# Kernel optimization log

Measured on AMD Instinct MI355X. Metric: run time of the kernel, lower is better.

Reference implementation:

```python
import jax, jax.numpy as jnp
import numpy as np

EMBED = 512
HEADS = 8
HEAD_DIM = EMBED // HEADS


def setup_inputs() -> dict:
    key = jax.random.key(0)
    ks = jax.random.split(key, 11)
    B, S, E = 2, 4096, EMBED
    scale = 1.0 / np.sqrt(E)
    inp = {
        "q": jax.random.normal(ks[0], (B, S, E), dtype=jnp.float32),
        "k": jax.random.normal(ks[1], (B, S, E), dtype=jnp.float32),
        "v": jax.random.normal(ks[2], (B, S, E), dtype=jnp.float32),
        # linear layer params (torch nn.Linear: y = x @ W.T + b)
        "Wq": jax.random.normal(ks[3], (E, E), dtype=jnp.float32) * scale,
        "bq": jnp.zeros((E,), dtype=jnp.float32),
        "Wk": jax.random.normal(ks[4], (E, E), dtype=jnp.float32) * scale,
        "bk": jnp.zeros((E,), dtype=jnp.float32),
        "Wv": jax.random.normal(ks[5], (E, E), dtype=jnp.float32) * scale,
        "bv": jnp.zeros((E,), dtype=jnp.float32),
        "Wo": jax.random.normal(ks[6], (E, E), dtype=jnp.float32) * scale,
        "bo": jnp.zeros((E,), dtype=jnp.float32),
    }
    return inp


def reference(q, k, v, Wq, bq, Wk, bk, Wv, bv, Wo, bo):
    B, Sq, E = q.shape
    Sk = k.shape[1]
    H, D = HEADS, HEAD_DIM
    # projections, split heads: [B, S, H, D]
    qh = (q @ Wq.T + bq).reshape(B, Sq, H, D)
    kh = (k @ Wk.T + bk).reshape(B, Sk, H, D)
    vh = (v @ Wv.T + bv).reshape(B, Sk, H, D)
    # full score matrix [B, H, Sq, Sk]; note: scaled by sqrt(embed_size), matching source
    scores = jnp.einsum('bqhe,bkhe->bhqk', qh, kh) / jnp.sqrt(jnp.float32(E))
    probs = jax.nn.softmax(scores, axis=-1)
    attn = jnp.einsum('bhql,blhd->bqhd', probs, vh)  # [B, Sq, H, D]
    concat = attn.reshape(B, Sq, E)
    return concat @ Wo.T + bo
```

## Files before the change

kernel.cpp:

```cpp
#include <hip/hip_runtime.h>
#include <hip/hip_bf16.h>

#define DEVFN __device__ __forceinline__

typedef __attribute__((ext_vector_type(8))) __bf16 bf16x8;
typedef __attribute__((ext_vector_type(4))) float f32x4;
typedef __attribute__((ext_vector_type(16))) float f32x16;

constexpr int E  = 512;
constexpr int S  = 4096;
constexpr int HD = 64;
constexpr int RT = 8192;

DEVFN unsigned int cvt_pk_bf16(float lo, float hi) {
  unsigned int r;
  asm("v_cvt_pk_bf16_f32 %0, %1, %2" : "=v"(r) : "v"(lo), "v"(hi));
  return r;
}
DEVFN void plswap(unsigned int& a, unsigned int& b) {
  asm("v_permlane32_swap_b32 %0, %1" : "+v"(a), "+v"(b));
}
DEVFN float ex2(float x) { return __builtin_amdgcn_exp2f(x); }

DEVFN unsigned short f2bf(float f) {
  union { float f; unsigned int u; } v; v.f = f;
  unsigned int u = v.u;
  return (unsigned short)((u + 0x7fffu + ((u >> 16) & 1u)) >> 16);
}

DEVFN f32x4 mfma16(bf16x8 a, bf16x8 b, f32x4 c) {
  return __builtin_amdgcn_mfma_f32_16x16x32_bf16(a, b, c, 0, 0, 0);
}
DEVFN f32x16 mfma32(bf16x8 a, bf16x8 b, f32x16 c) {
  return __builtin_amdgcn_mfma_f32_32x32x16_bf16(a, b, c, 0, 0, 0);
}

DEVFN uint4 pk8(const float4& a, const float4& b) {
  uint4 r;
  r.x = cvt_pk_bf16(a.x, a.y); r.y = cvt_pk_bf16(a.z, a.w);
  r.z = cvt_pk_bf16(b.x, b.y); r.w = cvt_pk_bf16(b.z, b.w);
  return r;
}
DEVFN bf16x8 asbf(uint4 u) { union { uint4 a; bf16x8 b; } c; c.a = u; return c.b; }

template<typename TIN, int OMODE>
DEVFN void gemm_body(const TIN* __restrict__ X, const float* __restrict__ W,
                     const float* __restrict__ bias, void* __restrict__ outp,
                     float scale, unsigned short (*Al)[72], unsigned short (*Bl)[72]) {
  const int bid0 = blockIdx.x;
  const int bid = ((bid0 & 7) << 5) | (bid0 >> 3);
  const int bm = bid >> 2, bn = bid & 3;
  const int tid = threadIdx.x;
  const int w = tid >> 6, lane = tid & 63;
  const int g = lane >> 4, ln = lane & 15;
  const int wm = w >> 2, wn = w & 3;
  const int r0 = bm * 128, n0 = bn * 128;
  const int srw = tid >> 2, sc0 = (tid & 3) * 16;

  f32x4 acc[4][2] = {};

  float4 af[4];
  uint4  au[2];
  float4 bp[4];

  auto loadA = [&](int k0) {
    if constexpr (sizeof(TIN) == 4) {
      const float* src = (const float*)X + (size_t)(r0 + srw) * E + k0 + sc0;
      #pragma unroll
      for (int i = 0; i < 4; ++i) af[i] = *(const float4*)(src + i * 4);
    } else {
      const unsigned short* src = (const unsigned short*)X + (size_t)(r0 + srw) * E + k0 + sc0;
      #pragma unroll
      for (int i = 0; i < 2; ++i) au[i] = *(const uint4*)(src + i * 8);
    }
  };
  auto loadB = [&](int k0) {
    const float* src = W + (size_t)(n0 + srw) * E + k0 + sc0;
    #pragma unroll
    for (int i = 0; i < 4; ++i) bp[i] = *(const float4*)(src + i * 4);
  };

  loadA(0); loadB(0);

  for (int k0 = 0; k0 < E; k0 += 64) {
    if constexpr (sizeof(TIN) == 4) {
      *(uint4*)&Al[srw][sc0]     = pk8(af[0], af[1]);
      *(uint4*)&Al[srw][sc0 + 8] = pk8(af[2], af[3]);
    } else {
      *(uint4*)&Al[srw][sc0]     = au[0];
      *(uint4*)&Al[srw][sc0 + 8] = au[1];
    }
    *(uint4*)&Bl[srw][sc0]     = pk8(bp[0], bp[1]);
    *(uint4*)&Bl[srw][sc0 + 8] = pk8(bp[2], bp[3]);
    __syncthreads();
    if (k0 + 64 < E) { loadA(k0 + 64); loadB(k0 + 64); }

    __builtin_amdgcn_s_setprio(1);
    #pragma unroll
    for (int kk = 0; kk < 2; ++kk) {
      bf16x8 afr[4], bfr[2];
      #pragma unroll
      for (int i = 0; i < 4; ++i)
        afr[i] = *(const bf16x8*)&Al[wm*64 + i*16 + ln][kk*32 + 8*g];
      #pragma unroll
      for (int j = 0; j < 2; ++j)
        bfr[j] = *(const bf16x8*)&Bl[wn*32 + j*16 + ln][kk*32 + 8*g];
      #pragma unroll
      for (int i = 0; i < 4; ++i)
        #pragma unroll
        for (int j = 0; j < 2; ++j)
          acc[i][j] = mfma16(afr[i], bfr[j], acc[i][j]);
    }
    __builtin_amdgcn_s_setprio(0);
    __syncthreads();
  }

  #pragma unroll
  for (int j = 0; j < 2; ++j) {
    const int gcol = n0 + wn*32 + j*16 + ln;
    const float bv = bias[gcol];
    #pragma unroll
    for (int i = 0; i < 4; ++i) {
      const int gr = r0 + wm*64 + i*16 + 4*g;
      #pragma unroll
      for (int r = 0; r < 4; ++r) {
        const float v = (acc[i][j][r] + bv) * scale;
        if constexpr (OMODE == 1)
          ((float*)outp)[(size_t)(gr + r) * E + gcol] = v;
        else if constexpr (OMODE == 0)
          ((unsigned short*)outp)[(size_t)(gr + r) * E + gcol] = f2bf(v);
        else
          ((unsigned short*)outp)[((size_t)((gr + r) >> 12) * E + gcol) * S + ((gr + r) & (S - 1))] = f2bf(v);
      }
    }
  }
}

__global__ __launch_bounds__(512) void gemm_qkv(const float* __restrict__ q,
    const float* __restrict__ k, const float* __restrict__ v,
    const float* __restrict__ Wq, const float* __restrict__ bq,
    const float* __restrict__ Wk, const float* __restrict__ bk,
    const float* __restrict__ Wv, const float* __restrict__ bv,
    unsigned short* qh, unsigned short* kh, unsigned short* vhT, float qscale) {
  __shared__ unsigned short Al[128][72];
  __shared__ unsigned short Bl[128][72];
  const int y = blockIdx.y;
  if (y == 0)      gemm_body<float, 0>(q, Wq, bq, qh, qscale, Al, Bl);
  else if (y == 1) gemm_body<float, 0>(k, Wk, bk, kh, 1.0f, Al, Bl);
  else             gemm_body<float, 2>(v, Wv, bv, vhT, 1.0f, Al, Bl);
}

__global__ __launch_bounds__(512) void gemm_o(const unsigned short* __restrict__ cc,
    const float* __restrict__ Wo, const float* __restrict__ bo, float* out) {
  __shared__ unsigned short Al[128][72];
  __shared__ unsigned short Bl[128][72];
  gemm_body<unsigned short, 1>(cc, Wo, bo, out, 1.0f, Al, Bl);
}

__global__ __launch_bounds__(512, 4) void attn_fwd(const unsigned short* __restrict__ qh,
                                                   const unsigned short* __restrict__ kh,
                                                   const unsigned short* __restrict__ vhT,
                                                   unsigned short* __restrict__ cc) {
  __shared__ unsigned short SM[2][4][64][72];

  const int bid = blockIdx.x;
  const int swz = (bid & 7) * 64 + (bid >> 3);
  const int bh = swz >> 5, qt = swz & 31;
  const int b = bh >> 3, h = bh & 7;

  const int tid = threadIdx.x;
  const int wv = tid >> 6, lane = tid & 63;
  const int half = wv >> 2, w4 = wv & 3;
  const int l31 = lane & 31, hi = lane >> 5;

  const unsigned short* qb = qh + (size_t)b * S * E + h * HD;
  const unsigned short* kb = kh + (size_t)b * S * E + h * HD;
  const unsigned short* vb = vhT + ((size_t)b * E + h * HD) * S;
  const int q0 = qt * 128 + w4 * 32;
  const int tbase = half * (S / 2);

  bf16x8 qf[4];
  #pragma unroll
  for (int kf = 0; kf < 4; ++kf)
    qf[kf] = *(const bf16x8*)(qb + (size_t)(q0 + l31) * E + kf*16 + 8*hi);

  f32x16 o0 = {}, o1 = {};
  float ml = 0.f, ll_par = 0.f;

  const int t256 = tid & 255;
  const int srow = t256 >> 2, sc0 = (t256 & 3) * 16;
  const unsigned short* kS = kb + (size_t)(tbase + srow) * E + sc0;
  const unsigned short* vS = vb + (size_t)srow * S + tbase + sc0;

  uint4 kr0 = *(const uint4*)kS, kr1 = *(const uint4*)(kS + 8);
  uint4 vr0 = *(const uint4*)vS, vr1 = *(const uint4*)(vS + 8);

  constexpr int NIT = S / 2 / 64;
  for (int it = 0; it < NIT; ++it) {
    unsigned short (*K_lds)[72] = SM[it & 1][2*half];
    unsigned short (*V_lds)[72] = SM[it & 1][2*half + 1];

    *(uint4*)&K_lds[srow][sc0]     = kr0;
    *(uint4*)&K_lds[srow][sc0 + 8] = kr1;
    *(uint4*)&V_lds[srow][sc0]     = vr0;
    *(uint4*)&V_lds[srow][sc0 + 8] = vr1;
    __syncthreads();

    if (it + 1 < NIT) {
      const unsigned short* kp = kS + (size_t)(it + 1) * 64 * E;
      const unsigned short* vp = vS + (it + 1) * 64;
      kr0 = *(const uint4*)kp; kr1 = *(const uint4*)(kp + 8);
      vr0 = *(const uint4*)vp; vr1 = *(const uint4*)(vp + 8);
    }

    const float negml = 0.f - ml;
    f32x16 s0, s1;
    #pragma unroll
    for (int r = 0; r < 16; ++r) { s0[r] = negml; s1[r] = negml; }
    __builtin_amdgcn_s_setprio(1);
    #pragma unroll
    for (int kf = 0; kf < 4; ++kf) {
      bf16x8 ka = *(const bf16x8*)&K_lds[l31]     [kf*16 + 8*hi];
      bf16x8 kc = *(const bf16x8*)&K_lds[32 + l31][kf*16 + 8*hi];
      s0 = mfma32(ka, qf[kf], s0);
      s1 = mfma32(kc, qf[kf], s1);
    }
    __builtin_amdgcn_s_setprio(0);

    float m0 = fmaxf(fmaxf(s0[0],  s0[1]),  s0[2]);
    float m1 = fmaxf(fmaxf(s0[3],  s0[4]),  s0[5]);
    float m2 = fmaxf(fmaxf(s0[6],  s0[7]),  s0[8]);
    float m3 = fmaxf(fmaxf(s0[9],  s0[10]), s0[11]);
    float m4 = fmaxf(fmaxf(s0[12], s0[13]), s0[14]);
    float m5 = fmaxf(fmaxf(s0[15], s1[0]),  s1[1]);
    float m6 = fmaxf(fmaxf(s1[2],  s1[3]),  s1[4]);
    float m7 = fmaxf(fmaxf(s1[5],  s1[6]),  s1[7]);
    float m8 = fmaxf(fmaxf(s1[8],  s1[9]),  s1[10]);
    float m9 = fmaxf(fmaxf(s1[11], s1[12]), s1[13]);
    float ma = fmaxf(s1[14], s1[15]);
    float tb0 = fmaxf(fmaxf(m0, m1), m2);
    float tb1 = fmaxf(fmaxf(m3, m4), m5);
    float tb2 = fmaxf(fmaxf(m6, m7), m8);
    float tm = fmaxf(fmaxf(tb0, tb1), fmaxf(tb2, fmaxf(m9, ma)));

    if (!__all(tm <= 8.f)) {
      tm = fmaxf(tm, __shfl_xor(tm, 32));
      const float delta = fmaxf(tm, 0.f);
      const float fr = ex2(-delta);
      ml += delta; ll_par *= fr;
      #pragma unroll
      for (int r = 0; r < 16; ++r) {
        o0[r] *= fr; o1[r] *= fr;
        s0[r] -= delta; s1[r] -= delta;
      }
    }

    float rs0 = 0.f, rs1 = 0.f;
    #pragma unroll
    for (int r = 0; r < 16; ++r) { s0[r] = ex2(s0[r]); rs0 += s0[r]; }
    #pragma unroll
    for (int r = 0; r < 16; ++r) { s1[r] = ex2(s1[r]); rs1 += s1[r]; }
    ll_par += rs0 + rs1;

    unsigned int a0 = cvt_pk_bf16(s0[0],  s0[1]),  a1 = cvt_pk_bf16(s0[2],  s0[3]);
    unsigned int a2 = cvt_pk_bf16(s0[4],  s0[5]),  a3 = cvt_pk_bf16(s0[6],  s0[7]);
    unsigned int a4 = cvt_pk_bf16(s0[8],  s0[9]),  a5 = cvt_pk_bf16(s0[10], s0[11]);
    unsigned int a6 = cvt_pk_bf16(s0[12], s0[13]), a7 = cvt_pk_bf16(s0[14], s0[15]);
    plswap(a0, a2); plswap(a1, a3); plswap(a4, a6); plswap(a5, a7);
    unsigned int c0 = cvt_pk_bf16(s1[0],  s1[1]),  c1 = cvt_pk_bf16(s1[2],  s1[3]);
    unsigned int c2 = cvt_pk_bf16(s1[4],  s1[5]),  c3 = cvt_pk_bf16(s1[6],  s1[7]);
    unsigned int c4 = cvt_pk_bf16(s1[8],  s1[9]),  c5 = cvt_pk_bf16(s1[10], s1[11]);
    unsigned int c6 = cvt_pk_bf16(s1[12], s1[13]), c7 = cvt_pk_bf16(s1[14], s1[15]);
    plswap(c0, c2); plswap(c1, c3); plswap(c4, c6); plswap(c5, c7);
    uint4 pa[4];
    pa[0] = uint4{a0, a1, a2, a3};
    pa[1] = uint4{a4, a5, a6, a7};
    pa[2] = uint4{c0, c1, c2, c3};
    pa[3] = uint4{c4, c5, c6, c7};

    __builtin_amdgcn_s_setprio(1);
    #pragma unroll
    for (int tf = 0; tf < 4; ++tf) {
      bf16x8 va = *(const bf16x8*)&V_lds[l31]     [tf*16 + 8*hi];
      bf16x8 vc = *(const bf16x8*)&V_lds[32 + l31][tf*16 + 8*hi];
      bf16x8 pf = asbf(pa[tf]);
      o0 = mfma32(va, pf, o0);
      o1 = mfma32(vc, pf, o1);
    }
    __builtin_amdgcn_s_setprio(0);
  }

  float ll = ll_par + __shfl_xor(ll_par, 32);

  __syncthreads();

  float* cb = (float*)SM;
  float* p = cb + (size_t)(w4 * 64 + lane) * 34;
  if (half) {
    #pragma unroll
    for (int r = 0; r < 16; ++r) { p[r] = o0[r]; p[16 + r] = o1[r]; }
    p[32] = ml; p[33] = ll;
  }
  __syncthreads();
  if (!half) {
    const float m2 = p[32], l2 = p[33];
    const float m = fmaxf(ml, m2);
    const float f1 = ex2(ml - m), f2 = ex2(m2 - m);
    ll = ll * f1 + l2 * f2;
    #pragma unroll
    for (int r = 0; r < 16; ++r) {
      o0[r] = o0[r] * f1 + p[r] * f2;
      o1[r] = o1[r] * f1 + p[16 + r] * f2;
    }

    const float inv = 1.0f / ll;
    const size_t rowb = (size_t)(b * S + q0 + l31) * E + h * HD;
    #pragma unroll
    for (int qd = 0; qd < 4; ++qd) {
      uint2 w0, w1;
      w0.x = cvt_pk_bf16(o0[4*qd]     * inv, o0[4*qd + 1] * inv);
      w0.y = cvt_pk_bf16(o0[4*qd + 2] * inv, o0[4*qd + 3] * inv);
      *(uint2*)&cc[rowb + 8*qd + 4*hi] = w0;
      w1.x = cvt_pk_bf16(o1[4*qd]     * inv, o1[4*qd + 1] * inv);
      w1.y = cvt_pk_bf16(o1[4*qd + 2] * inv, o1[4*qd + 3] * inv);
      *(uint2*)&cc[rowb + 32 + 8*qd + 4*hi] = w1;
    }
  }
}

extern "C" void kernel_launch(void* const* d_in, const int* in_sizes, int n_in,
                              void* d_out, int out_size, void* d_ws, size_t ws_size,
                              hipStream_t stream) {
  const float* q  = (const float*)d_in[0];
  const float* k  = (const float*)d_in[1];
  const float* v  = (const float*)d_in[2];
  const float* Wq = (const float*)d_in[3];
  const float* bq = (const float*)d_in[4];
  const float* Wk = (const float*)d_in[5];
  const float* bk = (const float*)d_in[6];
  const float* Wv = (const float*)d_in[7];
  const float* bv = (const float*)d_in[8];
  const float* Wo = (const float*)d_in[9];
  const float* bo = (const float*)d_in[10];
  float* out = (float*)d_out;

  unsigned short* qh  = (unsigned short*)d_ws;
  unsigned short* kh  = qh + (size_t)RT * E;
  unsigned short* vhT = kh + (size_t)RT * E;
  unsigned short* cc  = vhT + (size_t)RT * E;

  const float qscale = 1.4426950408889634f / 22.62741699796952f;

  gemm_qkv<<<dim3(256, 3), dim3(512), 0, stream>>>(q, k, v, Wq, bq, Wk, bk, Wv, bv,
                                                   qh, kh, vhT, qscale);
  attn_fwd<<<dim3(512), dim3(512), 0, stream>>>(qh, kh, vhT, cc);
  gemm_o<<<dim3(256), dim3(512), 0, stream>>>(cc, Wo, bo, out);
}
```

Baseline: 135.8 us.

## Double-buffer GEMM LDS tiles with BK=32 and drop second barrier

The projection GEMMs now use two LDS buffers with a K-step of 32 instead of one buffer with K-step 64. Each iteration writes into alternating buffers, so the trailing __syncthreads is removed and there is one barrier per step. The aim is to cut synchronization stalls and register pressure from prefetching. The cost is twice as many iterations and barriers in total, with less MFMA work per barrier. The single-barrier ping-pong relies on the two-buffer distance being enough to avoid overwriting a buffer still being read.

```diff
diff --git a/kernel.cpp b/kernel.cpp
--- a/kernel.cpp
+++ b/kernel.cpp
@@ -46,7 +46,8 @@
 template<typename TIN, int OMODE>
 DEVFN void gemm_body(const TIN* __restrict__ X, const float* __restrict__ W,
                      const float* __restrict__ bias, void* __restrict__ outp,
-                     float scale, unsigned short (*Al)[72], unsigned short (*Bl)[72]) {
+                     float scale,
+                     unsigned short (*Al)[128][40], unsigned short (*Bl)[128][40]) {
   const int bid0 = blockIdx.x;
   const int bid = ((bid0 & 7) << 5) | (bid0 >> 3);
   const int bm = bid >> 2, bn = bid & 3;
@@ -55,64 +56,58 @@
   const int g = lane >> 4, ln = lane & 15;
   const int wm = w >> 2, wn = w & 3;
   const int r0 = bm * 128, n0 = bn * 128;
-  const int srw = tid >> 2, sc0 = (tid & 3) * 16;
+  const int srw = tid >> 2, sc0 = (tid & 3) * 8;
 
   f32x4 acc[4][2] = {};
 
-  float4 af[4];
-  uint4  au[2];
-  float4 bp[4];
+  float4 af0, af1;
+  uint4  au;
+  float4 bp0, bp1;
 
   auto loadA = [&](int k0) {
     if constexpr (sizeof(TIN) == 4) {
       const float* src = (const float*)X + (size_t)(r0 + srw) * E + k0 + sc0;
-      #pragma unroll
-      for (int i = 0; i < 4; ++i) af[i] = *(const float4*)(src + i * 4);
+      af0 = *(const float4*)src;
+      af1 = *(const float4*)(src + 4);
     } else {
       const unsigned short* src = (const unsigned short*)X + (size_t)(r0 + srw) * E + k0 + sc0;
-      #pragma unroll
-      for (int i = 0; i < 2; ++i) au[i] = *(const uint4*)(src + i * 8);
+      au = *(const uint4*)src;
     }
   };
   auto loadB = [&](int k0) {
     const float* src = W + (size_t)(n0 + srw) * E + k0 + sc0;
-    #pragma unroll
-    for (int i = 0; i < 4; ++i) bp[i] = *(const float4*)(src + i * 4);
+    bp0 = *(const float4*)src;
+    bp1 = *(const float4*)(src + 4);
   };
 
   loadA(0); loadB(0);
 
-  for (int k0 = 0; k0 < E; k0 += 64) {
-    if constexpr (sizeof(TIN) == 4) {
-      *(uint4*)&Al[srw][sc0]     = pk8(af[0], af[1]);
-      *(uint4*)&Al[srw][sc0 + 8] = pk8(af[2], af[3]);
-    } else {
-      *(uint4*)&Al[srw][sc0]     = au[0];
-      *(uint4*)&Al[srw][sc0 + 8] = au[1];
-    }
-    *(uint4*)&Bl[srw][sc0]     = pk8(bp[0], bp[1]);
-    *(uint4*)&Bl[srw][sc0 + 8] = pk8(bp[2], bp[3]);
+  #pragma unroll 4
+  for (int it = 0; it < E / 32; ++it) {
+    const int p = it & 1;
+    if constexpr (sizeof(TIN) == 4)
+      *(uint4*)&Al[p][srw][sc0] = pk8(af0, af1);
+    else
+      *(uint4*)&Al[p][srw][sc0] = au;
+    *(uint4*)&Bl[p][srw][sc0] = pk8(bp0, bp1);
     __syncthreads();
-    if (k0 + 64 < E) { loadA(k0 + 64); loadB(k0 + 64); }
+
+    if (it + 1 < E / 32) { loadA((it + 1) * 32); loadB((it + 1) * 32); }
 
     __builtin_amdgcn_s_setprio(1);
-    #pragma unroll
-    for (int kk = 0; kk < 2; ++kk) {
-      bf16x8 afr[4], bfr[2];
-      #pragma unroll
-      for (int i = 0; i < 4; ++i)
-        afr[i] = *(const bf16x8*)&Al[wm*64 + i*16 + ln][kk*32 + 8*g];
+    bf16x8 afr[4], bfr[2];
+    #pragma unroll
+    for (int i = 0; i < 4; ++i)
+      afr[i] = *(const bf16x8*)&Al[p][wm*64 + i*16 + ln][8*g];
+    #pragma unroll
+    for (int j = 0; j < 2; ++j)
+      bfr[j] = *(const bf16x8*)&Bl[p][wn*32 + j*16 + ln][8*g];
+    #pragma unroll
+    for (int i = 0; i < 4; ++i)
       #pragma unroll
       for (int j = 0; j < 2; ++j)
-        bfr[j] = *(const bf16x8*)&Bl[wn*32 + j*16 + ln][kk*32 + 8*g];
-      #pragma unroll
-      for (int i = 0; i < 4; ++i)
-        #pragma unroll
-        for (int j = 0; j < 2; ++j)
-          acc[i][j] = mfma16(afr[i], bfr[j], acc[i][j]);
-    }
+        acc[i][j] = mfma16(afr[i], bfr[j], acc[i][j]);
     __builtin_amdgcn_s_setprio(0);
-    __syncthreads();
   }
 
   #pragma unroll
@@ -142,8 +137,8 @@
     const float* __restrict__ Wk, const float* __restrict__ bk,
     const float* __restrict__ Wv, const float* __restrict__ bv,
     unsigned short* qh, unsigned short* kh, unsigned short* vhT, float qscale) {
-  __shared__ unsigned short Al[128][72];
-  __shared__ unsigned short Bl[128][72];
+  __shared__ unsigned short Al[2][128][40];
+  __shared__ unsigned short Bl[2][128][40];
   const int y = blockIdx.y;
   if (y == 0)      gemm_body<float, 0>(q, Wq, bq, qh, qscale, Al, Bl);
   else if (y == 1) gemm_body<float, 0>(k, Wk, bk, kh, 1.0f, Al, Bl);
@@ -152,8 +147,8 @@
 
 __global__ __launch_bounds__(512) void gemm_o(const unsigned short* __restrict__ cc,
     const float* __restrict__ Wo, const float* __restrict__ bo, float* out) {
-  __shared__ unsigned short Al[128][72];
-  __shared__ unsigned short Bl[128][72];
+  __shared__ unsigned short Al[2][128][40];
+  __shared__ unsigned short Bl[2][128][40];
   gemm_body<unsigned short, 1>(cc, Wo, bo, out, 1.0f, Al, Bl);
 }
 
```

Result: faster. 127.7 us (-6.0%).
